# Kernel tuning notes

Hardware: AMD Instinct MI355X
Metric: run time of the kernel (lower is better)

## Reference

```python
import jax, jax.numpy as jnp
import numpy as np

# Model dims (GatedAttentionLayer of Qwen3.5 ANE hybrid stack)
C = 2048      # hidden_size
H = 16        # num_attention_heads
HK = 4        # num_key_value_heads
D = 128       # head_dim
ROT = 32      # rotary_dim = head_dim * partial_rotary_factor (0.25)
S = 1024      # sequence length (prefill)
CTX = 1024    # kv cache context length
N_ATTN = 6    # number of full-attention layers -> kv_cache leading dim 2*N_ATTN
EPS = 1e-6
ROPE_THETA = 1e7


def _rotate_half(x):
    h = x.shape[-1] // 2
    return jnp.concatenate([-x[..., h:], x[..., :h]], axis=-1)


def _rms_norm(x, w, eps=EPS):
    # Qwen3.5 convention: stored weight is (w - 1), applied as (1 + weight)
    r = jax.lax.rsqrt(jnp.mean(x * x, axis=-1, keepdims=True) + eps)
    return x * r * (1.0 + w)


def setup_inputs() -> dict:
    key = jax.random.key(0)
    ks = jax.random.split(key, 6)
    hidden_states = jax.random.normal(ks[0], (1, C, 1, S), jnp.float32)
    q_proj_w = jax.random.normal(ks[1], (H * 2 * D, C), jnp.float32) * 0.02  # q + gate
    k_proj_w = jax.random.normal(ks[2], (HK * D, C), jnp.float32) * 0.02
    v_proj_w = jax.random.normal(ks[3], (HK * D, C), jnp.float32) * 0.02
    o_proj_w = jax.random.normal(ks[4], (C, H * D), jnp.float32) * 0.02
    q_norm_w = jnp.zeros((D,), jnp.float32)
    k_norm_w = jnp.zeros((D,), jnp.float32)
    kv_cache = jnp.zeros((2 * N_ATTN, HK, CTX, D), jnp.float32)
    position_ids = jnp.arange(S, dtype=jnp.int32)
    # causal mask: 0 on/below diagonal, -1e9 above
    causal_mask = jnp.where(
        jnp.arange(CTX)[None, :] <= jnp.arange(S)[:, None], 0.0, -1e9
    ).astype(jnp.float32)[None, None]  # [1,1,S,CTX]
    # RoPE tables over rotary_dim
    inv_freq = 1.0 / (ROPE_THETA ** (jnp.arange(0, ROT, 2, dtype=jnp.float32) / ROT))
    t = jnp.arange(CTX, dtype=jnp.float32)
    freqs = jnp.outer(t, inv_freq)          # [CTX, ROT//2]
    emb = jnp.concatenate([freqs, freqs], -1)  # [CTX, ROT]
    cos_cached = jnp.cos(emb)
    sin_cached = jnp.sin(emb)
    return dict(hidden_states=hidden_states, q_proj_w=q_proj_w, k_proj_w=k_proj_w,
                v_proj_w=v_proj_w, o_proj_w=o_proj_w, q_norm_w=q_norm_w,
                k_norm_w=k_norm_w, kv_cache=kv_cache, causal_mask=causal_mask,
                position_ids=position_ids, cos_cached=cos_cached,
                sin_cached=sin_cached, attn_layer_idx=0)


def reference(hidden_states, q_proj_w, k_proj_w, v_proj_w, o_proj_w,
              q_norm_w, k_norm_w, kv_cache, causal_mask, position_ids,
              cos_cached, sin_cached, attn_layer_idx):
    x = hidden_states[0, :, 0, :]                     # [C, S]
    q_raw = q_proj_w @ x                              # [H*2D, S]  (1x1 Conv2d == GEMM)
    qg = q_raw.reshape(H, 2 * D, S)
    q = jnp.transpose(qg[:, :D, :], (0, 2, 1))        # [H, S, D]
    gate = jnp.transpose(qg[:, D:, :], (0, 2, 1))     # [H, S, D]
    k = jnp.transpose((k_proj_w @ x).reshape(HK, D, S), (0, 2, 1))  # [HK, S, D]
    v = jnp.transpose((v_proj_w @ x).reshape(HK, D, S), (0, 2, 1))  # [HK, S, D]

    q = _rms_norm(q, q_norm_w)
    k = _rms_norm(k, k_norm_w)

    cos = cos_cached[position_ids]   # [S, ROT]
    sin = sin_cached[position_ids]

    def rope(t):
        rot, pas = t[..., :ROT], t[..., ROT:]
        rot = rot * cos + _rotate_half(rot) * sin
        return jnp.concatenate([rot, pas], axis=-1)

    q, k = rope(q), rope(k)

    # prefill cache write at pos_start = position_ids[0]
    k_idx = 2 * attn_layer_idx
    v_idx = k_idx + 1
    pos_start = position_ids[0]
    kv_cache = jax.lax.dynamic_update_slice(kv_cache, k[None], (k_idx, 0, pos_start, 0))
    kv_cache = jax.lax.dynamic_update_slice(kv_cache, v[None], (v_idx, 0, pos_start, 0))

    g = H // HK  # GQA repeat (expand+reshape == contiguous repeat)
    k_full = jnp.repeat(kv_cache[k_idx], g, axis=0)   # [H, CTX, D]
    v_full = jnp.repeat(kv_cache[v_idx], g, axis=0)   # [H, CTX, D]

    scale = D ** -0.5
    attn = jnp.einsum('hsd,htd->hst', q, k_full) * scale + causal_mask[0]
    attn = jax.nn.softmax(attn, axis=-1)
    out = jnp.einsum('hst,htd->hsd', attn, v_full)    # [H, S, D]
    out = out * jax.nn.sigmoid(gate)
    out = jnp.transpose(out, (0, 2, 1)).reshape(H * D, S)
    output = (o_proj_w @ out)[None, :, None, :]       # [1, C, 1, S]
    return output
```

## Files before the change

### kernel.cpp

```cpp
#include <hip/hip_runtime.h>
#include <cstdint>

#define S_LEN 1024
#define C_DIM 2048
#define NH    16
#define NHK   4
#define HD    128
#define ROT   32
#define SCALE 0.08838834764831845f

typedef __bf16 bf16x8 __attribute__((ext_vector_type(8)));
typedef float floatx4 __attribute__((ext_vector_type(4)));
typedef float floatx16 __attribute__((ext_vector_type(16)));
typedef unsigned short ushortx8 __attribute__((ext_vector_type(8)));

__device__ __forceinline__ unsigned short f2bf(float f) {
  union { float f; uint32_t u; } x; x.f = f;
  uint32_t r = (x.u + 0x7fffu + ((x.u >> 16) & 1u)) >> 16;
  return (unsigned short)r;
}
__device__ __forceinline__ float bf2f(unsigned short v) {
  union { uint32_t u; float f; } x; x.u = (uint32_t)v << 16; return x.f;
}

__device__ __forceinline__ void async_copy16(const unsigned short* g, unsigned short* l) {
  __builtin_amdgcn_global_load_lds(
      (const __attribute__((address_space(1))) void*)g,
      (__attribute__((address_space(3))) void*)l,
      16, 0, 0);
}

#define WAIT_VM(N) asm volatile("s_waitcnt vmcnt(" #N ")" ::: "memory")

__device__ __forceinline__ void bar_lds_only() {
  asm volatile("s_waitcnt lgkmcnt(0)" ::: "memory");
  __builtin_amdgcn_s_barrier();
}

__device__ __forceinline__ int swz8(int row) { return (row ^ (row >> 3)) & 7; }

__global__ __launch_bounds__(256)
void prep_kernel(const float* __restrict__ qw, const float* __restrict__ kw,
                 const float* __restrict__ vw, const float* __restrict__ ow,
                 unsigned short* __restrict__ wout,
                 const float* __restrict__ x, unsigned short* __restrict__ xT) {
  __shared__ float t[32][33];
  int bid = blockIdx.x;
  if (bid < 14336) {
    const int NQ = 4096 * 2048 / 4, NK = 512 * 2048 / 4, NV = 512 * 2048 / 4;
    int i = bid * 256 + threadIdx.x;
    const float* src; int j;
    if (i < NQ) { src = qw; j = i; }
    else if (i < NQ + NK) { src = kw; j = i - NQ; }
    else if (i < NQ + NK + NV) { src = vw; j = i - NQ - NK; }
    else { src = ow; j = i - NQ - NK - NV; }
    float4 v = ((const float4*)src)[j];
    ushort4 o;
    o.x = f2bf(v.x); o.y = f2bf(v.y); o.z = f2bf(v.z); o.w = f2bf(v.w);
    ((ushort4*)wout)[i] = o;
  } else {
    int b2 = bid - 14336;
    int st = b2 & 31, ct = b2 >> 5;
    int c = threadIdx.x & 31, rq = threadIdx.x >> 5;
#pragma unroll
    for (int i = 0; i < 4; ++i) {
      int r = rq + i * 8;
      t[r][c] = x[(size_t)(ct * 32 + r) * S_LEN + st * 32 + c];
    }
    __syncthreads();
#pragma unroll
    for (int i = 0; i < 4; ++i) {
      int r = rq + i * 8;
      xT[(size_t)(st * 32 + r) * C_DIM + ct * 32 + c] = f2bf(t[c][r]);
    }
  }
}

__device__ __forceinline__ void norm_rope_epi4(
    floatx16 (&acc)[2], float (*pp)[64],
    const float* __restrict__ w, const int* __restrict__ pos_ids,
    const float* __restrict__ cosc, const float* __restrict__ sinc,
    unsigned short* __restrict__ outp,
    int wave, int lane, int wm, int scol0) {
  int l31 = lane & 31, half = lane >> 5;
#pragma unroll
  for (int ni = 0; ni < 2; ++ni) {
    float s = 0.f;
#pragma unroll
    for (int reg = 0; reg < 16; ++reg) { float v = acc[ni][reg]; s += v * v; }
    s += __shfl_xor(s, 32);
    if (half == 0) pp[wave][ni * 32 + l31] = s;
  }
  __syncthreads();
#pragma unroll
  for (int ni = 0; ni < 2; ++ni) {
    int ci = ni * 32 + l31;
    float tot = pp[0][ci] + pp[1][ci] + pp[2][ci] + pp[3][ci];
    float rn = rsqrtf(tot * (1.0f / 128.0f) + 1e-6f);
    int scol = scol0 + ni * 32 + l31;
    int pos = pos_ids[scol];
    bool rope = (wm == 0);
#pragma unroll
    for (int g = 0; g < 4; ++g) {
      int dbase = wm + half * 4 + g * 8;
      ushort4 o;
#pragma unroll
      for (int rr = 0; rr < 4; ++rr) {
        int reg = g * 4 + rr;
        int d = dbase + rr;
        float v = acc[ni][reg] * rn * (1.0f + w[d]);
        if (rope) {
          float cv = cosc[pos * ROT + d], sv = sinc[pos * ROT + d];
          int d2 = (d < 16) ? d + 16 : d - 16;
          float pv = acc[ni][reg ^ 8] * rn * (1.0f + w[d2]);
          v = v * cv + ((d < 16) ? -pv : pv) * sv;
        }
        ((unsigned short*)&o)[rr] = f2bf(v);
      }
      *(ushort4*)&outp[(size_t)scol * HD + dbase] = o;
    }
  }
}

#define STAGE_QKV4(B_, KT)                                                     \
  { _Pragma("unroll")                                                          \
    for (int i = 0; i < 4; ++i) {                                              \
      int row = wm + i * 8 + sr;                                               \
      async_copy16(Ag + (size_t)row * C_DIM + (KT) + (sc ^ swz8(row)) * 8,     \
                   &Asm[B_][(wm + i * 8) * 64]);                               \
    }                                                                          \
    _Pragma("unroll")                                                          \
    for (int i = 0; i < 2; ++i) {                                              \
      int row = wave * 16 + i * 8 + sr;                                        \
      async_copy16(Bg + (size_t)row * C_DIM + (KT) + (sc ^ swz8(row)) * 8,     \
                   &Bsm[B_][(wave * 16 + i * 8) * 64]);                        \
    } }

__global__ __launch_bounds__(256, 2)
void gemm_qkv_fused(const unsigned short* __restrict__ A,
                    const unsigned short* __restrict__ BT,
                    const float* __restrict__ qw, const float* __restrict__ kw,
                    const int* __restrict__ pos_ids,
                    const float* __restrict__ cosc, const float* __restrict__ sinc,
                    unsigned short* __restrict__ qb, unsigned short* __restrict__ kbuf,
                    unsigned short* __restrict__ vTb, unsigned short* __restrict__ sgb) {
  __shared__ unsigned short Asm[3][128 * 64];
  __shared__ unsigned short Bsm[3][64 * 64];
  __shared__ float pp[4][64];
  int tid = threadIdx.x, wave = tid >> 6, lane = tid & 63;
  int l31 = lane & 31, half = lane >> 5;
  int wm = wave * 32;
  int m0 = blockIdx.x * 128, n0 = blockIdx.y * 64;
  int sr = lane >> 3, sc = lane & 7;
  const unsigned short* Ag = A + (size_t)m0 * C_DIM;
  const unsigned short* Bg = BT + (size_t)n0 * C_DIM;
  int aswz = swz8(wm + l31);
  int bswz0 = swz8(l31), bswz1 = swz8(32 + l31);
  floatx16 acc[2];
  acc[0] = (floatx16)0.f; acc[1] = (floatx16)0.f;

  STAGE_QKV4(0, 0)
  STAGE_QKV4(1, 64)

  int b = 0;
  for (int t = 0; t < 32; ++t) {
    if (t < 31) { WAIT_VM(6); } else { WAIT_VM(0); }
    bar_lds_only();
    if (t < 30) {
      int bs = b + 2; if (bs >= 3) bs -= 3;
      STAGE_QKV4(bs, (t + 2) * 64)
    }
#pragma unroll
    for (int kb = 0; kb < 4; ++kb) {
      int c2 = (kb << 1) | half;
      bf16x8 av  = *(const bf16x8*)&Asm[b][(wm + l31) * 64 + ((c2 ^ aswz) << 3)];
      bf16x8 b0v = *(const bf16x8*)&Bsm[b][l31 * 64 + ((c2 ^ bswz0) << 3)];
      bf16x8 b1v = *(const bf16x8*)&Bsm[b][(32 + l31) * 64 + ((c2 ^ bswz1) << 3)];
      acc[0] = __builtin_amdgcn_mfma_f32_32x32x16_bf16(av, b0v, acc[0], 0, 0, 0);
      acc[1] = __builtin_amdgcn_mfma_f32_32x32x16_bf16(av, b1v, acc[1], 0, 0, 0);
    }
    ++b; if (b >= 3) b = 0;
  }

  int scol0 = n0;
  int ty = blockIdx.x;
  if (ty < 32) {
    int h = ty >> 1;
    if ((ty & 1) == 0) {
      norm_rope_epi4(acc, pp, qw, pos_ids, cosc, sinc,
                     qb + (size_t)h * S_LEN * HD, wave, lane, wm, scol0);
    } else {
#pragma unroll
      for (int ni = 0; ni < 2; ++ni) {
        int scol = scol0 + ni * 32 + l31;
#pragma unroll
        for (int g = 0; g < 4; ++g) {
          int dbase = wm + half * 4 + g * 8;
          ushort4 o;
#pragma unroll
          for (int rr = 0; rr < 4; ++rr)
            ((unsigned short*)&o)[rr] = f2bf(1.0f / (1.0f + __expf(-acc[ni][g * 4 + rr])));
          *(ushort4*)&sgb[((size_t)h * S_LEN + scol) * HD + dbase] = o;
        }
      }
    }
  } else if (ty < 36) {
    int hk = ty - 32;
    norm_rope_epi4(acc, pp, kw, pos_ids, cosc, sinc,
                   kbuf + (size_t)hk * S_LEN * HD, wave, lane, wm, scol0);
  } else {
    int hk = ty - 36;
#pragma unroll
    for (int ni = 0; ni < 2; ++ni)
#pragma unroll
      for (int reg = 0; reg < 16; ++reg) {
        int d = wm + (reg & 3) + 8 * (reg >> 2) + 4 * half;
        vTb[(size_t)hk * HD * S_LEN + (size_t)d * S_LEN + scol0 + ni * 32 + l31] =
            f2bf(acc[ni][reg]);
      }
  }
}

#define STAGE_O8(B_, KT)                                                       \
  { int rowA0 = r8;                                                            \
    async_copy16(Ag + (size_t)rowA0 * C_DIM + (KT) + (c8 ^ swz8(rowA0)) * 8,   \
                 &Asm[B_][(wave * 8) * 64]);                                   \
    int rowA1 = r8 + 64;                                                       \
    async_copy16(Ag + (size_t)rowA1 * C_DIM + (KT) + (c8 ^ swz8(rowA1)) * 8,   \
                 &Asm[B_][(64 + wave * 8) * 64]);                              \
    int rowB = r8;                                                             \
    async_copy16(Bg + (size_t)rowB * C_DIM + (KT) + (c8 ^ swz8(rowB)) * 8,     \
                 &Bsm[B_][(wave * 8) * 64]); }

__global__ __launch_bounds__(512, 2)
void gemm_oproj(const unsigned short* __restrict__ A,
                const unsigned short* __restrict__ BT,
                float* __restrict__ C) {
  __shared__ unsigned short Asm[3][128 * 64];
  __shared__ unsigned short Bsm[3][64 * 64];
  int tid = threadIdx.x, wave = tid >> 6, lane = tid & 63;
  int l31 = lane & 31, half = lane >> 5;
  int wm = (wave & 3) * 32, wn = (wave >> 2) * 32;
  int m0 = blockIdx.x * 128, n0 = blockIdx.y * 64;
  int r8 = tid >> 3, c8 = tid & 7;
  int aswz = swz8(wm + l31), bswz = swz8(wn + l31);
  const unsigned short* Ag = A + (size_t)m0 * C_DIM;
  const unsigned short* Bg = BT + (size_t)n0 * C_DIM;
  floatx16 acc = (floatx16)0.f;

  STAGE_O8(0, 0)
  STAGE_O8(1, 64)

  int b = 0;
  for (int t = 0; t < 32; ++t) {
    if (t < 31) { WAIT_VM(3); } else { WAIT_VM(0); }
    bar_lds_only();
    if (t < 30) {
      int bs = b + 2; if (bs >= 3) bs -= 3;
      STAGE_O8(bs, (t + 2) * 64)
    }
#pragma unroll
    for (int kb = 0; kb < 4; ++kb) {
      int ca = (((kb << 1) | half) ^ aswz) << 3;
      int cb = (((kb << 1) | half) ^ bswz) << 3;
      bf16x8 av = *(const bf16x8*)&Asm[b][(wm + l31) * 64 + ca];
      bf16x8 bv = *(const bf16x8*)&Bsm[b][(wn + l31) * 64 + cb];
      acc = __builtin_amdgcn_mfma_f32_32x32x16_bf16(av, bv, acc, 0, 0, 0);
    }
    ++b; if (b >= 3) b = 0;
  }

#pragma unroll
  for (int reg = 0; reg < 16; ++reg) {
    int row = m0 + wm + (reg & 3) + 8 * (reg >> 2) + 4 * half;
    C[(size_t)row * S_LEN + n0 + wn + l31] = acc[reg];
  }
}

__global__ __launch_bounds__(256)
void attn_kernel(const unsigned short* __restrict__ qb,
                 const unsigned short* __restrict__ kbuf,
                 const unsigned short* __restrict__ vTb,
                 float* __restrict__ pm, float* __restrict__ pl,
                 float* __restrict__ pO0, float* __restrict__ pO1) {
  __shared__ __align__(16) unsigned short Ks[64 * 128];
  __shared__ __align__(16) unsigned short Vs[128 * 64];
  __shared__ __align__(16) unsigned short Ps[4][16][72];
  int h = blockIdx.x, qt = blockIdx.y, ch = blockIdx.z;
  int t0 = ch * 4;
  if (t0 > qt) return;
  int t1 = min(qt, t0 + 3);
  int s0 = qt * 64;
  int hk = h >> 2;
  int tid = threadIdx.x, wave = tid >> 6, lane = tid & 63;
  int l16 = lane & 15, quad = lane >> 4;
  int lsw = l16 & 7;

  const unsigned short* qg = qb + ((size_t)(h * S_LEN + s0 + wave * 16 + l16)) * HD;
  bf16x8 qfr[4];
#pragma unroll
  for (int kb = 0; kb < 4; ++kb)
    qfr[kb] = *(const bf16x8*)(qg + kb * 32 + quad * 8);

  float m_r[4], l_r[4];
#pragma unroll
  for (int r = 0; r < 4; ++r) { m_r[r] = -1e30f; l_r[r] = 0.f; }
  floatx4 acc_o[8];
#pragma unroll
  for (int i = 0; i < 8; ++i) acc_o[i] = (floatx4)0.f;
  int srow_base = s0 + wave * 16 + quad * 4;

  const unsigned short* kg0 = kbuf + (size_t)hk * S_LEN * HD;
  const unsigned short* vg0 = vTb + (size_t)hk * HD * S_LEN;

  int kr4 = lane >> 4, kc16 = lane & 15;
  int vr8 = lane >> 3, vc8 = lane & 7;

  for (int t = t0; t <= t1; ++t) {
    int jt = t * 64;
#pragma unroll
    for (int i = 0; i < 4; ++i) {
      int rbase = wave * 16 + i * 4;
      int row = rbase + kr4;
      int cs = kc16 ^ (row & 7);
      async_copy16(kg0 + (size_t)(jt + row) * HD + cs * 8, Ks + rbase * 128);
    }
#pragma unroll
    for (int i = 0; i < 4; ++i) {
      int rbase = wave * 32 + i * 8;
      int row = rbase + vr8;
      int cs = vc8 ^ (row & 7);
      async_copy16(vg0 + (size_t)row * S_LEN + jt + cs * 8, Vs + rbase * 64);
    }
    __syncthreads();

    floatx4 acc_s[4];
#pragma unroll
    for (int ni = 0; ni < 4; ++ni) acc_s[ni] = (floatx4)0.f;
#pragma unroll
    for (int kb = 0; kb < 4; ++kb) {
#pragma unroll
      for (int ni = 0; ni < 4; ++ni) {
        int cl = (kb * 4 + quad) ^ lsw;
        bf16x8 bk = *(const bf16x8*)&Ks[(ni * 16 + l16) * 128 + cl * 8];
        acc_s[ni] = __builtin_amdgcn_mfma_f32_16x16x32_bf16(qfr[kb], bk, acc_s[ni], 0, 0, 0);
      }
    }

    bool diag = (t == qt);
    float alpha[4];
#pragma unroll
    for (int r = 0; r < 4; ++r) {
      float scv[4];
      float mx = -1e30f;
#pragma unroll
      for (int ni = 0; ni < 4; ++ni) {
        float sv = acc_s[ni][r] * SCALE;
        if (diag) {
          int jg = jt + ni * 16 + l16;
          if (jg > srow_base + r) sv = -1e30f;
        }
        scv[ni] = sv;
        mx = fmaxf(mx, sv);
      }
#pragma unroll
      for (int off = 8; off; off >>= 1) mx = fmaxf(mx, __shfl_xor(mx, off, 16));
      float mnew = fmaxf(m_r[r], mx);
      float psv = 0.f;
#pragma unroll
      for (int ni = 0; ni < 4; ++ni) {
        float pv = (scv[ni] > -1e29f) ? __expf(scv[ni] - mnew) : 0.f;
        Ps[wave][quad * 4 + r][ni * 16 + l16] = f2bf(pv);
        psv += pv;
      }
#pragma unroll
      for (int off = 8; off; off >>= 1) psv += __shfl_xor(psv, off, 16);
      alpha[r] = __expf(m_r[r] - mnew);
      m_r[r] = mnew;
      l_r[r] = l_r[r] * alpha[r] + psv;
    }
#pragma unroll
    for (int i = 0; i < 8; ++i)
#pragma unroll
      for (int r = 0; r < 4; ++r) acc_o[i][r] *= alpha[r];
    __threadfence_block();

#pragma unroll
    for (int kb2 = 0; kb2 < 2; ++kb2) {
      bf16x8 ap = *(const bf16x8*)&Ps[wave][l16][kb2 * 32 + quad * 8];
#pragma unroll
      for (int ni2 = 0; ni2 < 8; ++ni2) {
        int cl = (kb2 * 4 + quad) ^ lsw;
        bf16x8 bv = *(const bf16x8*)&Vs[(ni2 * 16 + l16) * 64 + cl * 8];
        acc_o[ni2] = __builtin_amdgcn_mfma_f32_16x16x32_bf16(ap, bv, acc_o[ni2], 0, 0, 0);
      }
    }
    __syncthreads();
  }

  size_t pmbase = ((size_t)(h * 16 + qt) * 4 + ch) * 64;
  float* pOp = (ch < 2) ? pO0 + ((size_t)(h * 16 + qt) * 2 + ch) * 8192
                        : pO1 + ((size_t)(h * 16 + qt) * 2 + (ch - 2)) * 8192;
#pragma unroll
  for (int r = 0; r < 4; ++r) {
    int rrow = wave * 16 + quad * 4 + r;
    if (l16 == 0) { pm[pmbase + rrow] = m_r[r]; pl[pmbase + rrow] = l_r[r]; }
#pragma unroll
    for (int ni2 = 0; ni2 < 8; ++ni2)
      pOp[rrow * 128 + ni2 * 16 + l16] = acc_o[ni2][r];
  }
}

__global__ __launch_bounds__(256)
void attn_merge(const float* __restrict__ pm, const float* __restrict__ pl,
                const float* __restrict__ pO0, const float* __restrict__ pO1,
                const unsigned short* __restrict__ sgb,
                unsigned short* __restrict__ outT) {
  int h = blockIdx.x, qt = blockIdx.y;
  int vc = (qt >> 2) + 1;
  size_t base = (size_t)(h * 16 + qt) * 4;
  int lane32 = threadIdx.x & 31, rb = threadIdx.x >> 5;
  int d = lane32 * 4;
#pragma unroll
  for (int rr = 0; rr < 8; ++rr) {
    int row = rr * 8 + rb;
    float M = -1e30f;
    for (int c = 0; c < vc; ++c) M = fmaxf(M, pm[(base + c) * 64 + row]);
    float L = 0.f;
    floatx4 acc = (floatx4)0.f;
    for (int c = 0; c < vc; ++c) {
      float w = __expf(pm[(base + c) * 64 + row] - M);
      L += w * pl[(base + c) * 64 + row];
      const float* Op = (c < 2) ? pO0 + ((size_t)(h * 16 + qt) * 2 + c) * 8192
                                : pO1 + ((size_t)(h * 16 + qt) * 2 + (c - 2)) * 8192;
      floatx4 o = *(const floatx4*)&Op[row * 128 + d];
#pragma unroll
      for (int j = 0; j < 4; ++j) acc[j] += w * o[j];
    }
    float inv = 1.0f / L;
    int s = qt * 64 + row;
    ushort4 sg4 = *(const ushort4*)&sgb[((size_t)h * S_LEN + s) * HD + d];
    ushort4 out4;
#pragma unroll
    for (int j = 0; j < 4; ++j)
      ((unsigned short*)&out4)[j] = f2bf(acc[j] * inv * bf2f(((unsigned short*)&sg4)[j]));
    *(ushort4*)&outT[(size_t)s * (NH * HD) + h * HD + d] = out4;
  }
}

extern "C" void kernel_launch(void* const* d_in, const int* in_sizes, int n_in,
                              void* d_out, int out_size, void* d_ws, size_t ws_size,
                              hipStream_t stream) {
  const float* hs       = (const float*)d_in[0];
  const float* q_proj_w = (const float*)d_in[1];
  const float* k_proj_w = (const float*)d_in[2];
  const float* v_proj_w = (const float*)d_in[3];
  const float* o_proj_w = (const float*)d_in[4];
  const float* q_norm_w = (const float*)d_in[5];
  const float* k_norm_w = (const float*)d_in[6];
  const int*   pos_ids  = (const int*)d_in[9];
  const float* cos_c    = (const float*)d_in[10];
  const float* sin_c    = (const float*)d_in[11];
  float* out = (float*)d_out;

  char* ws = (char*)d_ws;
  unsigned short* wqkv = (unsigned short*)(ws + 0);
  unsigned short* wo   = (unsigned short*)(ws + 20971520);
  unsigned short* xT   = (unsigned short*)(ws + 29360128);
  unsigned short* qb   = (unsigned short*)(ws + 33554432);
  unsigned short* kbuf = (unsigned short*)(ws + 37748736);
  unsigned short* vTb  = (unsigned short*)(ws + 38797312);
  unsigned short* sgb  = (unsigned short*)(ws + 39845888);
  unsigned short* aoT  = (unsigned short*)(ws + 44040192);
  float*          pO0  = (float*)(ws + 0);
  float*          pO1  = (float*)(ws + 48234496);
  float*          pm   = (float*)(ws + 65011712);
  float*          pl   = (float*)(ws + 65273856);

  prep_kernel<<<14336 + 2048, 256, 0, stream>>>(q_proj_w, k_proj_w, v_proj_w, o_proj_w,
                                                wqkv, hs, xT);
  gemm_qkv_fused<<<dim3(40, 16), 256, 0, stream>>>(wqkv, xT, q_norm_w, k_norm_w,
                                                   pos_ids, cos_c, sin_c,
                                                   qb, kbuf, vTb, sgb);
  attn_kernel<<<dim3(16, 16, 4), 256, 0, stream>>>(qb, kbuf, vTb, pm, pl, pO0, pO1);
  attn_merge<<<dim3(16, 16), 256, 0, stream>>>(pm, pl, pO0, pO1, sgb, aoT);
  gemm_oproj<<<dim3(16, 16), 512, 0, stream>>>(wo, aoT, out);
}
```

Before: 266.7 us.

## Switch QKV and O-proj GEMMs to double-buffered LDS with smaller o-proj tiles

The QKV GEMM drops from triple to double buffering, cutting LDS use so three blocks can share a CU. The prefetch now issues after compute, behind a barrier. The O-proj GEMM is reshaped from 128x64 tiles with 8 waves to 64x64 tiles with 2 waves, each computing two 32x32 outputs, and the grid doubles to 512 blocks for more parallelism across CUs. The trade-off is less load/compute overlap from the shallower pipeline and an extra barrier per k-step.

```diff
diff --git a/kernel.cpp b/kernel.cpp
--- a/kernel.cpp
+++ b/kernel.cpp
@@ -136,7 +136,7 @@
                    &Bsm[B_][(wave * 16 + i * 8) * 64]);                        \
     } }
 
-__global__ __launch_bounds__(256, 2)
+__global__ __launch_bounds__(256, 3)
 void gemm_qkv_fused(const unsigned short* __restrict__ A,
                     const unsigned short* __restrict__ BT,
                     const float* __restrict__ qw, const float* __restrict__ kw,
@@ -144,8 +144,8 @@
                     const float* __restrict__ cosc, const float* __restrict__ sinc,
                     unsigned short* __restrict__ qb, unsigned short* __restrict__ kbuf,
                     unsigned short* __restrict__ vTb, unsigned short* __restrict__ sgb) {
-  __shared__ unsigned short Asm[3][128 * 64];
-  __shared__ unsigned short Bsm[3][64 * 64];
+  __shared__ unsigned short Asm[2][128 * 64];
+  __shared__ unsigned short Bsm[2][64 * 64];
   __shared__ float pp[4][64];
   int tid = threadIdx.x, wave = tid >> 6, lane = tid & 63;
   int l31 = lane & 31, half = lane >> 5;
@@ -162,14 +162,10 @@
   STAGE_QKV4(0, 0)
   STAGE_QKV4(1, 64)
 
-  int b = 0;
   for (int t = 0; t < 32; ++t) {
+    int b = t & 1;
     if (t < 31) { WAIT_VM(6); } else { WAIT_VM(0); }
-    bar_lds_only();
-    if (t < 30) {
-      int bs = b + 2; if (bs >= 3) bs -= 3;
-      STAGE_QKV4(bs, (t + 2) * 64)
-    }
+    __builtin_amdgcn_s_barrier();
 #pragma unroll
     for (int kb = 0; kb < 4; ++kb) {
       int c2 = (kb << 1) | half;
@@ -179,7 +175,8 @@
       acc[0] = __builtin_amdgcn_mfma_f32_32x32x16_bf16(av, b0v, acc[0], 0, 0, 0);
       acc[1] = __builtin_amdgcn_mfma_f32_32x32x16_bf16(av, b1v, acc[1], 0, 0, 0);
     }
-    ++b; if (b >= 3) b = 0;
+    bar_lds_only();
+    if (t < 30) STAGE_QKV4(b, (t + 2) * 64)
   }
 
   int scol0 = n0;
@@ -221,60 +218,65 @@
   }
 }
 
-#define STAGE_O8(B_, KT)                                                       \
-  { int rowA0 = r8;                                                            \
-    async_copy16(Ag + (size_t)rowA0 * C_DIM + (KT) + (c8 ^ swz8(rowA0)) * 8,   \
-                 &Asm[B_][(wave * 8) * 64]);                                   \
-    int rowA1 = r8 + 64;                                                       \
-    async_copy16(Ag + (size_t)rowA1 * C_DIM + (KT) + (c8 ^ swz8(rowA1)) * 8,   \
-                 &Asm[B_][(64 + wave * 8) * 64]);                              \
-    int rowB = r8;                                                             \
-    async_copy16(Bg + (size_t)rowB * C_DIM + (KT) + (c8 ^ swz8(rowB)) * 8,     \
-                 &Bsm[B_][(wave * 8) * 64]); }
-
-__global__ __launch_bounds__(512, 2)
+#define STAGE_O2(B_, KT)                                                       \
+  { _Pragma("unroll")                                                          \
+    for (int i = 0; i < 4; ++i) {                                              \
+      int row = wm + i * 8 + sr;                                               \
+      async_copy16(Ag + (size_t)row * C_DIM + (KT) + (sc ^ swz8(row)) * 8,     \
+                   &Asm[B_][(wm + i * 8) * 64]);                               \
+    }                                                                          \
+    _Pragma("unroll")                                                          \
+    for (int i = 0; i < 4; ++i) {                                              \
+      int row = wm + i * 8 + sr;                                               \
+      async_copy16(Bg + (size_t)row * C_DIM + (KT) + (sc ^ swz8(row)) * 8,     \
+                   &Bsm[B_][(wm + i * 8) * 64]);                               \
+    } }
+
+__global__ __launch_bounds__(128, 2)
 void gemm_oproj(const unsigned short* __restrict__ A,
                 const unsigned short* __restrict__ BT,
                 float* __restrict__ C) {
-  __shared__ unsigned short Asm[3][128 * 64];
-  __shared__ unsigned short Bsm[3][64 * 64];
+  __shared__ unsigned short Asm[2][64 * 64];
+  __shared__ unsigned short Bsm[2][64 * 64];
   int tid = threadIdx.x, wave = tid >> 6, lane = tid & 63;
   int l31 = lane & 31, half = lane >> 5;
-  int wm = (wave & 3) * 32, wn = (wave >> 2) * 32;
-  int m0 = blockIdx.x * 128, n0 = blockIdx.y * 64;
-  int r8 = tid >> 3, c8 = tid & 7;
-  int aswz = swz8(wm + l31), bswz = swz8(wn + l31);
+  int wm = wave * 32;
+  int m0 = blockIdx.x * 64, n0 = blockIdx.y * 64;
+  int sr = lane >> 3, sc = lane & 7;
   const unsigned short* Ag = A + (size_t)m0 * C_DIM;
   const unsigned short* Bg = BT + (size_t)n0 * C_DIM;
-  floatx16 acc = (floatx16)0.f;
-
-  STAGE_O8(0, 0)
-  STAGE_O8(1, 64)
-
-  int b = 0;
+  int aswz = swz8(wm + l31);
+  int bswz0 = swz8(l31), bswz1 = swz8(32 + l31);
+  floatx16 acc[2];
+  acc[0] = (floatx16)0.f; acc[1] = (floatx16)0.f;
+
+  STAGE_O2(0, 0)
+  STAGE_O2(1, 64)
+
   for (int t = 0; t < 32; ++t) {
-    if (t < 31) { WAIT_VM(3); } else { WAIT_VM(0); }
+    int b = t & 1;
+    if (t < 31) { WAIT_VM(8); } else { WAIT_VM(0); }
+    __builtin_amdgcn_s_barrier();
+#pragma unroll
+    for (int kb = 0; kb < 4; ++kb) {
+      int c2 = (kb << 1) | half;
+      bf16x8 av  = *(const bf16x8*)&Asm[b][(wm + l31) * 64 + ((c2 ^ aswz) << 3)];
+      bf16x8 b0v = *(const bf16x8*)&Bsm[b][l31 * 64 + ((c2 ^ bswz0) << 3)];
+      bf16x8 b1v = *(const bf16x8*)&Bsm[b][(32 + l31) * 64 + ((c2 ^ bswz1) << 3)];
+      acc[0] = __builtin_amdgcn_mfma_f32_32x32x16_bf16(av, b0v, acc[0], 0, 0, 0);
+      acc[1] = __builtin_amdgcn_mfma_f32_32x32x16_bf16(av, b1v, acc[1], 0, 0, 0);
+    }
     bar_lds_only();
-    if (t < 30) {
-      int bs = b + 2; if (bs >= 3) bs -= 3;
-      STAGE_O8(bs, (t + 2) * 64)
-    }
-#pragma unroll
-    for (int kb = 0; kb < 4; ++kb) {
-      int ca = (((kb << 1) | half) ^ aswz) << 3;
-      int cb = (((kb << 1) | half) ^ bswz) << 3;
-      bf16x8 av = *(const bf16x8*)&Asm[b][(wm + l31) * 64 + ca];
-      bf16x8 bv = *(const bf16x8*)&Bsm[b][(wn + l31) * 64 + cb];
-      acc = __builtin_amdgcn_mfma_f32_32x32x16_bf16(av, bv, acc, 0, 0, 0);
-    }
-    ++b; if (b >= 3) b = 0;
-  }
-
-#pragma unroll
-  for (int reg = 0; reg < 16; ++reg) {
-    int row = m0 + wm + (reg & 3) + 8 * (reg >> 2) + 4 * half;
-    C[(size_t)row * S_LEN + n0 + wn + l31] = acc[reg];
-  }
+    if (t < 30) STAGE_O2(b, (t + 2) * 64)
+  }
+
+#pragma unroll
+  for (int ni = 0; ni < 2; ++ni)
+#pragma unroll
+    for (int reg = 0; reg < 16; ++reg) {
+      int row = m0 + wm + (reg & 3) + 8 * (reg >> 2) + 4 * half;
+      C[(size_t)row * S_LEN + n0 + ni * 32 + l31] = acc[ni][reg];
+    }
 }
 
 __global__ __launch_bounds__(256)
@@ -484,5 +486,5 @@
                                                    qb, kbuf, vTb, sgb);
   attn_kernel<<<dim3(16, 16, 4), 256, 0, stream>>>(qb, kbuf, vTb, pm, pl, pO0, pO1);
   attn_merge<<<dim3(16, 16), 256, 0, stream>>>(pm, pl, pO0, pO1, sgb, aoT);
-  gemm_oproj<<<dim3(16, 16), 512, 0, stream>>>(wo, aoT, out);
-}
+  gemm_oproj<<<dim3(32, 16), 128, 0, stream>>>(wo, aoT, out);
+}
```

Measured after the change: 231.4 us (median of 2 runs). -13.2%, faster.
